# Performance work log

Hardware: AMD Instinct MI355X
Metric: run time of the kernel (lower is better)

## Reference

```python
import jax, jax.numpy as jnp
import numpy as np

M, N, D = 8, 50000, 256  # n_relations, nodes, d_model


def setup_inputs() -> dict:
    key = jax.random.key(0)
    ks = jax.random.split(key, 6)
    s = 0.02
    return {
        "zs": jax.random.normal(ks[0], (M, N, D), jnp.float32),
        # W_beta: Linear(M*D -> M), stored as [in, out]
        "Wb": jax.random.normal(ks[1], (M * D, M), jnp.float32) * s,
        "bb": jnp.zeros((M,), jnp.float32),
        # per-relation Linear(D -> D) stacks, stored [M, in, out]
        "Wmax": jax.random.normal(ks[2], (M, D, D), jnp.float32) * s,
        "bmax": jnp.zeros((M, D), jnp.float32),
        "Wphi": jax.random.normal(ks[3], (M, D, D), jnp.float32) * s,
        "bphi": jnp.zeros((M, D), jnp.float32),
        # W_c: Linear(3D -> D)
        "Wc": jax.random.normal(ks[4], (3 * D, D), jnp.float32) * s,
        "bc": jnp.zeros((D,), jnp.float32),
        # LayerNorm affine params
        "gamma": jnp.ones((D,), jnp.float32),
        "beta": jnp.zeros((D,), jnp.float32),
    }


def reference(zs, Wb, bb, Wmax, bmax, Wphi, bphi, Wc, bc, gamma, beta):
    Mr, Nn, Dd = zs.shape
    # --- sum branch: gated softmax mixture over relations ---
    cat = jnp.transpose(zs, (1, 0, 2)).reshape(Nn, Mr * Dd)  # [N, M*D] (no pad: M == n_max)
    gate = jax.nn.softmax(cat @ Wb + bb, axis=-1)            # [N, M]
    z_sum = jnp.einsum('nm,mnd->nd', gate, zs)               # [N, D]
    # --- max branch: per-relation linear then elementwise max over relations ---
    proj = jnp.einsum('mnd,mde->mne', zs, Wmax) + bmax[:, None, :]  # [M, N, D]
    z_max = proj.max(axis=0)
    # --- agr branch: sum_{i<j} phi_i*phi_j = 0.5*((sum phi)^2 - sum phi^2) ---
    phis = jnp.einsum('mnd,mde->mne', zs, Wphi) + bphi[:, None, :]  # [M, N, D]
    s1 = phis.sum(axis=0)
    z_agr = 0.5 * (s1 * s1 - (phis * phis).sum(axis=0))
    # --- combine + LayerNorm ---
    z = jnp.concatenate([z_sum, z_max, z_agr], axis=-1) @ Wc + bc   # [N, D]
    mu = z.mean(axis=-1, keepdims=True)
    var = z.var(axis=-1, keepdims=True)
    return (z - mu) / jnp.sqrt(var + 1e-5) * gamma + beta
```

## Files before the change

### kernel.cpp

```cpp
#include <hip/hip_runtime.h>

typedef unsigned short u16;
typedef unsigned int   u32;
typedef __attribute__((ext_vector_type(8))) __bf16 bf16x8;
typedef __attribute__((ext_vector_type(4))) float  f32x4;

#define MREL  8
#define DDIM  256
#define TROWS 32

#define WPHI_B 1024
#define WB_B   2048
#define WC_B   2112
#define NBLK   2496

__device__ __forceinline__ u16 f2bf(float x) {
  u32 u = __float_as_uint(x);
  u += 0x7fffu + ((u >> 16) & 1u);
  return (u16)(u >> 16);
}
__device__ __forceinline__ float bf2f(u16 x) {
  return __uint_as_float((u32)x << 16);
}

union U16x8 { u16 u[8]; uint4 q; bf16x8 v; };

#define SLOT(q, lr, ks) ((q)*16 + ((((lr) ^ (ks)) ^ ((q) << 1)) & 15))

#define MFMA16 __builtin_amdgcn_mfma_f32_16x16x32_bf16

#define BARRIER() do { \
  asm volatile("s_waitcnt lgkmcnt(0)" ::: "memory"); \
  __builtin_amdgcn_s_barrier(); \
  asm volatile("" ::: "memory"); \
} while (0)

__global__ __launch_bounds__(256) void swizzle_kernel(
    const float* __restrict__ Wmax, const float* __restrict__ Wphi,
    const float* __restrict__ Wb,   const float* __restrict__ Wc,
    u16* __restrict__ ws)
{
  int sb   = blockIdx.x * 4 + (threadIdx.x >> 6);
  int lane = threadIdx.x & 63;
  int quad = lane >> 4, c16 = lane & 15;
  U16x8 o;
  if (sb < WB_B) {
    const float* W = (sb < WPHI_B) ? Wmax : Wphi;
    int b = sb & 1023;
    int m = b >> 7, r = b & 127;
    int ct = r >> 3, ks = r & 7;
    const float* src = W + ((size_t)m * DDIM + (size_t)(ks * 32 + quad * 8)) * DDIM
                         + ct * 16 + c16;
    #pragma unroll
    for (int j = 0; j < 8; ++j) o.u[j] = f2bf(src[j * DDIM]);
  } else if (sb < WC_B) {
    int ksg = sb - WB_B;
    int kbase = ksg * 32 + quad * 8;
    if (c16 < 8) {
      #pragma unroll
      for (int j = 0; j < 8; ++j) o.u[j] = f2bf(Wb[(size_t)(kbase + j) * 8 + c16]);
    } else {
      o.q = make_uint4(0, 0, 0, 0);
    }
  } else {
    int r = sb - WC_B;
    int ct = r / 24, ks = r % 24;
    const float* src = Wc + (size_t)(ks * 32 + quad * 8) * DDIM + ct * 16 + c16;
    #pragma unroll
    for (int j = 0; j < 8; ++j) o.u[j] = f2bf(src[j * DDIM]);
  }
  *(uint4*)(ws + (size_t)sb * 512 + lane * 8) = o.q;
}

__global__ __launch_bounds__(512, 2) void fused_kernel(
    const float* __restrict__ zs,   const float* __restrict__ bb,
    const float* __restrict__ bmax, const float* __restrict__ bphi,
    const float* __restrict__ bc,   const float* __restrict__ gma,
    const float* __restrict__ bta,  const u16* __restrict__ ws,
    float* __restrict__ out, int N)
{
  const int tid  = threadIdx.x;
  const int lane = tid & 63;
  const int w    = tid >> 6;
  const int quad = lane >> 4;
  const int c16  = lane & 15;
  const int n0   = blockIdx.x * TROWS;
  const int st_row = tid >> 4;
  const int t15    = tid & 15;

  __shared__ __align__(16) u16 s_tile[MREL * 8192];
  __shared__ float s_lpart[8][TROWS][8];
  __shared__ float s_gate[TROWS][8];
  __shared__ float s_ln1[TROWS][8];
  __shared__ float s_ln2[TROWS][8];
  __shared__ float s_mrs[TROWS][2];

  const f32x4 vz = {0.f, 0.f, 0.f, 0.f};
  f32x4 zmx[2][2], s1v[2][2], s2v[2][2];
  #pragma unroll
  for (int rt = 0; rt < 2; ++rt)
    #pragma unroll
    for (int ct = 0; ct < 2; ++ct) {
      zmx[rt][ct] = (f32x4){-3e38f, -3e38f, -3e38f, -3e38f};
      s1v[rt][ct] = vz; s2v[rt][ct] = vz;
    }
  f32x4 lf0 = vz, lf1 = vz;

  const int g_row = n0 + st_row;
  const int st_lr = st_row & 15, st_rt = st_row >> 4;
  const float* zbase = zs + (size_t)g_row * DDIM + t15 * 4;

  float4 Fa[4], Fb[4];
  auto issue = [&](int m, float4* F) {
    if (g_row < N) {
      const float* p = zbase + (size_t)m * N * DDIM;
      #pragma unroll
      for (int k = 0; k < 4; ++k) F[k] = *(const float4*)(p + k * 64);
    } else {
      #pragma unroll
      for (int k = 0; k < 4; ++k) F[k] = make_float4(0.f, 0.f, 0.f, 0.f);
    }
  };
  auto wtile = [&](int m, const float4* F) {
    u16* tile = s_tile + m * 8192;
    #pragma unroll
    for (int k = 0; k < 4; ++k) {
      int c0 = k * 64 + t15 * 4;
      int ks = c0 >> 5, q = (c0 >> 3) & 3, j = c0 & 7;
      u32 lo = (u32)f2bf(F[k].x) | ((u32)f2bf(F[k].y) << 16);
      u32 hi = (u32)f2bf(F[k].z) | ((u32)f2bf(F[k].w) << 16);
      *(uint2*)(tile + (st_rt * 8 + ks) * 512 + SLOT(q, st_lr, ks) * 8 + j) =
          make_uint2(lo, hi);
    }
  };

  auto compute = [&](int m) {
    const u16* tile = s_tile + m * 8192;
    float bm0 = bmax[m * DDIM + (w * 2 + 0) * 16 + c16];
    float bm1 = bmax[m * DDIM + (w * 2 + 1) * 16 + c16];
    float bp0 = bphi[m * DDIM + (w * 2 + 0) * 16 + c16];
    float bp1 = bphi[m * DDIM + (w * 2 + 1) * 16 + c16];
    {
      U16x8 bg, a0, a1;
      bg.q = *(const uint4*)(ws + (size_t)(WB_B + m * 8 + w) * 512 + lane * 8);
      int so = SLOT(quad, c16, w) * 8;
      a0.q = *(const uint4*)(tile + w * 512 + so);
      a1.q = *(const uint4*)(tile + (8 + w) * 512 + so);
      lf0 = MFMA16(a0.v, bg.v, lf0, 0, 0, 0);
      lf1 = MFMA16(a1.v, bg.v, lf1, 0, 0, 0);
    }
    f32x4 pa[2][2];
    #pragma unroll
    for (int rt = 0; rt < 2; ++rt)
      #pragma unroll
      for (int ct = 0; ct < 2; ++ct) pa[rt][ct] = vz;
    {
      uint4 B[8][2];
      #pragma unroll
      for (int ks = 0; ks < 8; ++ks) {
        B[ks][0] = *(const uint4*)(ws + (size_t)(m * 128 + (w * 2 + 0) * 8 + ks) * 512 + lane * 8);
        B[ks][1] = *(const uint4*)(ws + (size_t)(m * 128 + (w * 2 + 1) * 8 + ks) * 512 + lane * 8);
      }
      #pragma unroll
      for (int ks = 0; ks < 8; ++ks) {
        U16x8 a0, a1, b0, b1;
        int so = SLOT(quad, c16, ks) * 8;
        a0.q = *(const uint4*)(tile + ks * 512 + so);
        a1.q = *(const uint4*)(tile + (8 + ks) * 512 + so);
        b0.q = B[ks][0]; b1.q = B[ks][1];
        pa[0][0] = MFMA16(a0.v, b0.v, pa[0][0], 0, 0, 0);
        pa[0][1] = MFMA16(a0.v, b1.v, pa[0][1], 0, 0, 0);
        pa[1][0] = MFMA16(a1.v, b0.v, pa[1][0], 0, 0, 0);
        pa[1][1] = MFMA16(a1.v, b1.v, pa[1][1], 0, 0, 0);
      }
      #pragma unroll
      for (int rt = 0; rt < 2; ++rt)
        #pragma unroll
        for (int r = 0; r < 4; ++r) {
          zmx[rt][0][r] = fmaxf(zmx[rt][0][r], pa[rt][0][r] + bm0);
          zmx[rt][1][r] = fmaxf(zmx[rt][1][r], pa[rt][1][r] + bm1);
        }
    }
    #pragma unroll
    for (int rt = 0; rt < 2; ++rt)
      #pragma unroll
      for (int ct = 0; ct < 2; ++ct) pa[rt][ct] = vz;
    {
      uint4 B[8][2];
      #pragma unroll
      for (int ks = 0; ks < 8; ++ks) {
        B[ks][0] = *(const uint4*)(ws + (size_t)(WPHI_B + m * 128 + (w * 2 + 0) * 8 + ks) * 512 + lane * 8);
        B[ks][1] = *(const uint4*)(ws + (size_t)(WPHI_B + m * 128 + (w * 2 + 1) * 8 + ks) * 512 + lane * 8);
      }
      #pragma unroll
      for (int ks = 0; ks < 8; ++ks) {
        U16x8 a0, a1, b0, b1;
        int so = SLOT(quad, c16, ks) * 8;
        a0.q = *(const uint4*)(tile + ks * 512 + so);
        a1.q = *(const uint4*)(tile + (8 + ks) * 512 + so);
        b0.q = B[ks][0]; b1.q = B[ks][1];
        pa[0][0] = MFMA16(a0.v, b0.v, pa[0][0], 0, 0, 0);
        pa[0][1] = MFMA16(a0.v, b1.v, pa[0][1], 0, 0, 0);
        pa[1][0] = MFMA16(a1.v, b0.v, pa[1][0], 0, 0, 0);
        pa[1][1] = MFMA16(a1.v, b1.v, pa[1][1], 0, 0, 0);
      }
      #pragma unroll
      for (int rt = 0; rt < 2; ++rt)
        #pragma unroll
        for (int r = 0; r < 4; ++r) {
          float v0 = pa[rt][0][r] + bp0;
          float v1 = pa[rt][1][r] + bp1;
          s1v[rt][0][r] += v0; s2v[rt][0][r] += v0 * v0;
          s1v[rt][1][r] += v1; s2v[rt][1][r] += v1 * v1;
        }
    }
  };

  issue(0, Fa);
  for (int m = 0; m < MREL; m += 2) {
    issue(m + 1, Fb);
    wtile(m, Fa);
    BARRIER();
    compute(m);
    if (m + 2 < MREL) issue(m + 2, Fa);
    wtile(m + 1, Fb);
    BARRIER();
    compute(m + 1);
  }

  if (c16 < 8) {
    #pragma unroll
    for (int r = 0; r < 4; ++r) {
      s_lpart[w][quad * 4 + r][c16]      = lf0[r];
      s_lpart[w][16 + quad * 4 + r][c16] = lf1[r];
    }
  }
  __syncthreads();
  if (tid < TROWS) {
    float lg[8]; float mx = -1e30f;
    #pragma unroll
    for (int mm = 0; mm < 8; ++mm) {
      float v = bb[mm];
      #pragma unroll
      for (int ww = 0; ww < 8; ++ww) v += s_lpart[ww][tid][mm];
      lg[mm] = v; mx = fmaxf(mx, v);
    }
    float s = 0.f;
    #pragma unroll
    for (int mm = 0; mm < 8; ++mm) { lg[mm] = __expf(lg[mm] - mx); s += lg[mm]; }
    float inv = 1.f / s;
    #pragma unroll
    for (int mm = 0; mm < 8; ++mm) s_gate[tid][mm] = lg[mm] * inv;
  }
  __syncthreads();

  float zsum[16];
  #pragma unroll
  for (int i = 0; i < 16; ++i) zsum[i] = 0.f;
  const int z_ks = t15 >> 1;
  const int z_q0 = (t15 & 1) * 2;
  const int z_base = (st_rt * 8 + z_ks) * 512;
  const int z_so0 = z_base + SLOT(z_q0, st_lr, z_ks) * 8;
  const int z_so1 = z_base + SLOT(z_q0 + 1, st_lr, z_ks) * 8;
  #pragma unroll
  for (int m = 0; m < MREL; ++m) {
    float g = s_gate[st_row][m];
    const u16* tile = s_tile + m * 8192;
    U16x8 v0, v1;
    v0.q = *(const uint4*)(tile + z_so0);
    v1.q = *(const uint4*)(tile + z_so1);
    #pragma unroll
    for (int j = 0; j < 8; ++j) {
      zsum[j]     += g * bf2f(v0.u[j]);
      zsum[8 + j] += g * bf2f(v1.u[j]);
    }
  }
  __syncthreads();

  {
    U16x8 p0, p1;
    #pragma unroll
    for (int j = 0; j < 8; ++j) { p0.u[j] = f2bf(zsum[j]); p1.u[j] = f2bf(zsum[8 + j]); }
    *(uint4*)(s_tile + z_so0) = p0.q;
    *(uint4*)(s_tile + z_so1) = p1.q;
  }
  #pragma unroll
  for (int ct = 0; ct < 2; ++ct) {
    int col = (w * 2 + ct) * 16 + c16;
    int ks = col >> 5, q = (col >> 3) & 3, j = col & 7;
    #pragma unroll
    for (int rt = 0; rt < 2; ++rt)
      #pragma unroll
      for (int r = 0; r < 4; ++r) {
        int lr = quad * 4 + r;
        s_tile[8192 + (rt * 8 + ks) * 512 + SLOT(q, lr, ks) * 8 + j] = f2bf(zmx[rt][ct][r]);
      }
  }
  #pragma unroll
  for (int ct = 0; ct < 2; ++ct) {
    int col = (w * 2 + ct) * 16 + c16;
    int ks = col >> 5, q = (col >> 3) & 3, j = col & 7;
    #pragma unroll
    for (int rt = 0; rt < 2; ++rt)
      #pragma unroll
      for (int r = 0; r < 4; ++r) {
        int lr = quad * 4 + r;
        float za = 0.5f * (s1v[rt][ct][r] * s1v[rt][ct][r] - s2v[rt][ct][r]);
        s_tile[16384 + (rt * 8 + ks) * 512 + SLOT(q, lr, ks) * 8 + j] = f2bf(za);
      }
  }
  __syncthreads();

  f32x4 oc[2][2];
  #pragma unroll
  for (int rt = 0; rt < 2; ++rt)
    #pragma unroll
    for (int ct = 0; ct < 2; ++ct) oc[rt][ct] = vz;
  #pragma unroll
  for (int p = 0; p < 3; ++p) {
    const u16* pb = s_tile + p * 8192;
    uint4 B[8][2];
    #pragma unroll
    for (int ks = 0; ks < 8; ++ks) {
      B[ks][0] = *(const uint4*)(ws + (size_t)(WC_B + (w * 2 + 0) * 24 + p * 8 + ks) * 512 + lane * 8);
      B[ks][1] = *(const uint4*)(ws + (size_t)(WC_B + (w * 2 + 1) * 24 + p * 8 + ks) * 512 + lane * 8);
    }
    #pragma unroll
    for (int ks = 0; ks < 8; ++ks) {
      U16x8 a0, a1, b0, b1;
      int so = SLOT(quad, c16, ks) * 8;
      a0.q = *(const uint4*)(pb + ks * 512 + so);
      a1.q = *(const uint4*)(pb + (8 + ks) * 512 + so);
      b0.q = B[ks][0]; b1.q = B[ks][1];
      oc[0][0] = MFMA16(a0.v, b0.v, oc[0][0], 0, 0, 0);
      oc[0][1] = MFMA16(a0.v, b1.v, oc[0][1], 0, 0, 0);
      oc[1][0] = MFMA16(a1.v, b0.v, oc[1][0], 0, 0, 0);
      oc[1][1] = MFMA16(a1.v, b1.v, oc[1][1], 0, 0, 0);
    }
  }

  #pragma unroll
  for (int ct = 0; ct < 2; ++ct) {
    float bcv = bc[(w * 2 + ct) * 16 + c16];
    #pragma unroll
    for (int rt = 0; rt < 2; ++rt)
      #pragma unroll
      for (int r = 0; r < 4; ++r) oc[rt][ct][r] += bcv;
  }
  float ps[2][4], pss[2][4];
  #pragma unroll
  for (int rt = 0; rt < 2; ++rt)
    #pragma unroll
    for (int r = 0; r < 4; ++r) {
      float a = oc[rt][0][r], b = oc[rt][1][r];
      ps[rt][r]  = a + b;
      pss[rt][r] = a * a + b * b;
    }
  #pragma unroll
  for (int off = 1; off < 16; off <<= 1) {
    #pragma unroll
    for (int rt = 0; rt < 2; ++rt)
      #pragma unroll
      for (int r = 0; r < 4; ++r) {
        ps[rt][r]  += __shfl_xor(ps[rt][r], off);
        pss[rt][r] += __shfl_xor(pss[rt][r], off);
      }
  }
  if (c16 == 0) {
    #pragma unroll
    for (int rt = 0; rt < 2; ++rt)
      #pragma unroll
      for (int r = 0; r < 4; ++r) s_ln1[rt * 16 + quad * 4 + r][w] = ps[rt][r];
  }
  if (c16 == 1) {
    #pragma unroll
    for (int rt = 0; rt < 2; ++rt)
      #pragma unroll
      for (int r = 0; r < 4; ++r) s_ln2[rt * 16 + quad * 4 + r][w] = pss[rt][r];
  }
  __syncthreads();
  if (tid < TROWS) {
    float s = 0.f, ss = 0.f;
    #pragma unroll
    for (int ww = 0; ww < 8; ++ww) { s += s_ln1[tid][ww]; ss += s_ln2[tid][ww]; }
    float mu  = s * (1.0f / 256.0f);
    float var = ss * (1.0f / 256.0f) - mu * mu;
    s_mrs[tid][0] = mu;
    s_mrs[tid][1] = rsqrtf(var + 1e-5f);
  }
  __syncthreads();
  #pragma unroll
  for (int ct = 0; ct < 2; ++ct) {
    int col = (w * 2 + ct) * 16 + c16;
    float g = gma[col], b = bta[col];
    #pragma unroll
    for (int rt = 0; rt < 2; ++rt)
      #pragma unroll
      for (int r = 0; r < 4; ++r) {
        int row = rt * 16 + quad * 4 + r;
        int grow = n0 + row;
        if (grow < N) {
          float mu = s_mrs[row][0], rs = s_mrs[row][1];
          out[(size_t)grow * DDIM + col] = (oc[rt][ct][r] - mu) * rs * g + b;
        }
      }
  }
}

extern "C" void kernel_launch(void* const* d_in, const int* in_sizes, int n_in,
                              void* d_out, int out_size, void* d_ws, size_t ws_size,
                              hipStream_t stream) {
  const float* zs   = (const float*)d_in[0];
  const float* Wb   = (const float*)d_in[1];
  const float* bb   = (const float*)d_in[2];
  const float* Wmax = (const float*)d_in[3];
  const float* bmax = (const float*)d_in[4];
  const float* Wphi = (const float*)d_in[5];
  const float* bphi = (const float*)d_in[6];
  const float* Wc   = (const float*)d_in[7];
  const float* bc   = (const float*)d_in[8];
  const float* gma  = (const float*)d_in[9];
  const float* bta  = (const float*)d_in[10];
  float* out = (float*)d_out;
  u16* ws = (u16*)d_ws;

  int N = in_sizes[0] / (MREL * DDIM);

  swizzle_kernel<<<NBLK / 4, 256, 0, stream>>>(Wmax, Wphi, Wb, Wc, ws);
  int grid = (N + TROWS - 1) / TROWS;
  fused_kernel<<<grid, 512, 0, stream>>>(zs, bb, bmax, bphi, bc, gma, bta, ws, out, N);
}
```

Measured before the change: 813.9 us.

## Double block to 1024 threads, one column tile per wave, move prefetch into compute

The fused kernel now runs 16 waves per block instead of 8. Each wave owns one 16-column output tile instead of two, which halves per-thread accumulators and B-fragment registers. The staging loads become 32 bytes per thread with a single 16-byte LDS store, and the next relation's global load is issued inside compute after the Wphi fragments are fetched, to overlap latency. LDS use per block is unchanged, so occupancy is still limited by shared memory. The extra waves give more latency hiding, but also add barrier cost and duplicate B-fragment loads across more waves.

```diff
diff --git a/kernel.cpp b/kernel.cpp
--- a/kernel.cpp
+++ b/kernel.cpp
@@ -72,7 +72,7 @@
   *(uint4*)(ws + (size_t)sb * 512 + lane * 8) = o.q;
 }
 
-__global__ __launch_bounds__(512, 2) void fused_kernel(
+__global__ __launch_bounds__(1024, 4) void fused_kernel(
     const float* __restrict__ zs,   const float* __restrict__ bb,
     const float* __restrict__ bmax, const float* __restrict__ bphi,
     const float* __restrict__ bc,   const float* __restrict__ gma,
@@ -85,62 +85,56 @@
   const int quad = lane >> 4;
   const int c16  = lane & 15;
   const int n0   = blockIdx.x * TROWS;
-  const int st_row = tid >> 4;
-  const int t15    = tid & 15;
+  const int st_row = tid >> 5;
+  const int s32    = tid & 31;
 
   __shared__ __align__(16) u16 s_tile[MREL * 8192];
   __shared__ float s_lpart[8][TROWS][8];
   __shared__ float s_gate[TROWS][8];
-  __shared__ float s_ln1[TROWS][8];
-  __shared__ float s_ln2[TROWS][8];
+  __shared__ float s_ln1[TROWS][16];
+  __shared__ float s_ln2[TROWS][16];
   __shared__ float s_mrs[TROWS][2];
 
   const f32x4 vz = {0.f, 0.f, 0.f, 0.f};
-  f32x4 zmx[2][2], s1v[2][2], s2v[2][2];
-  #pragma unroll
-  for (int rt = 0; rt < 2; ++rt)
-    #pragma unroll
-    for (int ct = 0; ct < 2; ++ct) {
-      zmx[rt][ct] = (f32x4){-3e38f, -3e38f, -3e38f, -3e38f};
-      s1v[rt][ct] = vz; s2v[rt][ct] = vz;
-    }
+  f32x4 zmx[2], s1v[2], s2v[2];
+  #pragma unroll
+  for (int rt = 0; rt < 2; ++rt) {
+    zmx[rt] = (f32x4){-3e38f, -3e38f, -3e38f, -3e38f};
+    s1v[rt] = vz; s2v[rt] = vz;
+  }
   f32x4 lf0 = vz, lf1 = vz;
 
   const int g_row = n0 + st_row;
   const int st_lr = st_row & 15, st_rt = st_row >> 4;
-  const float* zbase = zs + (size_t)g_row * DDIM + t15 * 4;
-
-  float4 Fa[4], Fb[4];
+  const int st_ks = s32 >> 2, st_q = s32 & 3;
+  const int st_off = (st_rt * 8 + st_ks) * 512 + SLOT(st_q, st_lr, st_ks) * 8;
+  const float* zbase = zs + (size_t)g_row * DDIM + s32 * 8;
+
+  float4 Fa[2], Fb[2];
   auto issue = [&](int m, float4* F) {
     if (g_row < N) {
       const float* p = zbase + (size_t)m * N * DDIM;
-      #pragma unroll
-      for (int k = 0; k < 4; ++k) F[k] = *(const float4*)(p + k * 64);
+      F[0] = *(const float4*)p;
+      F[1] = *(const float4*)(p + 4);
     } else {
-      #pragma unroll
-      for (int k = 0; k < 4; ++k) F[k] = make_float4(0.f, 0.f, 0.f, 0.f);
+      F[0] = make_float4(0.f, 0.f, 0.f, 0.f);
+      F[1] = make_float4(0.f, 0.f, 0.f, 0.f);
     }
   };
   auto wtile = [&](int m, const float4* F) {
-    u16* tile = s_tile + m * 8192;
-    #pragma unroll
-    for (int k = 0; k < 4; ++k) {
-      int c0 = k * 64 + t15 * 4;
-      int ks = c0 >> 5, q = (c0 >> 3) & 3, j = c0 & 7;
-      u32 lo = (u32)f2bf(F[k].x) | ((u32)f2bf(F[k].y) << 16);
-      u32 hi = (u32)f2bf(F[k].z) | ((u32)f2bf(F[k].w) << 16);
-      *(uint2*)(tile + (st_rt * 8 + ks) * 512 + SLOT(q, st_lr, ks) * 8 + j) =
-          make_uint2(lo, hi);
-    }
+    U16x8 pk;
+    pk.u[0] = f2bf(F[0].x); pk.u[1] = f2bf(F[0].y);
+    pk.u[2] = f2bf(F[0].z); pk.u[3] = f2bf(F[0].w);
+    pk.u[4] = f2bf(F[1].x); pk.u[5] = f2bf(F[1].y);
+    pk.u[6] = f2bf(F[1].z); pk.u[7] = f2bf(F[1].w);
+    *(uint4*)(s_tile + m * 8192 + st_off) = pk.q;
   };
 
-  auto compute = [&](int m) {
+  auto compute = [&](int m, int mnext, float4* Fn) {
     const u16* tile = s_tile + m * 8192;
-    float bm0 = bmax[m * DDIM + (w * 2 + 0) * 16 + c16];
-    float bm1 = bmax[m * DDIM + (w * 2 + 1) * 16 + c16];
-    float bp0 = bphi[m * DDIM + (w * 2 + 0) * 16 + c16];
-    float bp1 = bphi[m * DDIM + (w * 2 + 1) * 16 + c16];
-    {
+    float bm = bmax[m * DDIM + w * 16 + c16];
+    float bp = bphi[m * DDIM + w * 16 + c16];
+    if (w < 8) {
       U16x8 bg, a0, a1;
       bg.q = *(const uint4*)(ws + (size_t)(WB_B + m * 8 + w) * 512 + lane * 8);
       int so = SLOT(quad, c16, w) * 8;
@@ -149,86 +143,67 @@
       lf0 = MFMA16(a0.v, bg.v, lf0, 0, 0, 0);
       lf1 = MFMA16(a1.v, bg.v, lf1, 0, 0, 0);
     }
-    f32x4 pa[2][2];
-    #pragma unroll
-    for (int rt = 0; rt < 2; ++rt)
-      #pragma unroll
-      for (int ct = 0; ct < 2; ++ct) pa[rt][ct] = vz;
+    f32x4 p0, p1;
+    p0 = vz; p1 = vz;
     {
-      uint4 B[8][2];
+      uint4 B[8];
+      #pragma unroll
+      for (int ks = 0; ks < 8; ++ks)
+        B[ks] = *(const uint4*)(ws + (size_t)(m * 128 + w * 8 + ks) * 512 + lane * 8);
       #pragma unroll
       for (int ks = 0; ks < 8; ++ks) {
-        B[ks][0] = *(const uint4*)(ws + (size_t)(m * 128 + (w * 2 + 0) * 8 + ks) * 512 + lane * 8);
-        B[ks][1] = *(const uint4*)(ws + (size_t)(m * 128 + (w * 2 + 1) * 8 + ks) * 512 + lane * 8);
-      }
-      #pragma unroll
-      for (int ks = 0; ks < 8; ++ks) {
-        U16x8 a0, a1, b0, b1;
+        U16x8 a0, a1, b;
         int so = SLOT(quad, c16, ks) * 8;
         a0.q = *(const uint4*)(tile + ks * 512 + so);
         a1.q = *(const uint4*)(tile + (8 + ks) * 512 + so);
-        b0.q = B[ks][0]; b1.q = B[ks][1];
-        pa[0][0] = MFMA16(a0.v, b0.v, pa[0][0], 0, 0, 0);
-        pa[0][1] = MFMA16(a0.v, b1.v, pa[0][1], 0, 0, 0);
-        pa[1][0] = MFMA16(a1.v, b0.v, pa[1][0], 0, 0, 0);
-        pa[1][1] = MFMA16(a1.v, b1.v, pa[1][1], 0, 0, 0);
-      }
-      #pragma unroll
-      for (int rt = 0; rt < 2; ++rt)
-        #pragma unroll
-        for (int r = 0; r < 4; ++r) {
-          zmx[rt][0][r] = fmaxf(zmx[rt][0][r], pa[rt][0][r] + bm0);
-          zmx[rt][1][r] = fmaxf(zmx[rt][1][r], pa[rt][1][r] + bm1);
-        }
-    }
-    #pragma unroll
-    for (int rt = 0; rt < 2; ++rt)
-      #pragma unroll
-      for (int ct = 0; ct < 2; ++ct) pa[rt][ct] = vz;
+        b.q = B[ks];
+        p0 = MFMA16(a0.v, b.v, p0, 0, 0, 0);
+        p1 = MFMA16(a1.v, b.v, p1, 0, 0, 0);
+      }
+      #pragma unroll
+      for (int r = 0; r < 4; ++r) {
+        zmx[0][r] = fmaxf(zmx[0][r], p0[r] + bm);
+        zmx[1][r] = fmaxf(zmx[1][r], p1[r] + bm);
+      }
+    }
+    p0 = vz; p1 = vz;
     {
-      uint4 B[8][2];
+      uint4 B[8];
+      #pragma unroll
+      for (int ks = 0; ks < 8; ++ks)
+        B[ks] = *(const uint4*)(ws + (size_t)(WPHI_B + m * 128 + w * 8 + ks) * 512 + lane * 8);
+      if (mnext >= 0) issue(mnext, Fn);
       #pragma unroll
       for (int ks = 0; ks < 8; ++ks) {
-        B[ks][0] = *(const uint4*)(ws + (size_t)(WPHI_B + m * 128 + (w * 2 + 0) * 8 + ks) * 512 + lane * 8);
-        B[ks][1] = *(const uint4*)(ws + (size_t)(WPHI_B + m * 128 + (w * 2 + 1) * 8 + ks) * 512 + lane * 8);
-      }
-      #pragma unroll
-      for (int ks = 0; ks < 8; ++ks) {
-        U16x8 a0, a1, b0, b1;
+        U16x8 a0, a1, b;
         int so = SLOT(quad, c16, ks) * 8;
         a0.q = *(const uint4*)(tile + ks * 512 + so);
         a1.q = *(const uint4*)(tile + (8 + ks) * 512 + so);
-        b0.q = B[ks][0]; b1.q = B[ks][1];
-        pa[0][0] = MFMA16(a0.v, b0.v, pa[0][0], 0, 0, 0);
-        pa[0][1] = MFMA16(a0.v, b1.v, pa[0][1], 0, 0, 0);
-        pa[1][0] = MFMA16(a1.v, b0.v, pa[1][0], 0, 0, 0);
-        pa[1][1] = MFMA16(a1.v, b1.v, pa[1][1], 0, 0, 0);
-      }
-      #pragma unroll
-      for (int rt = 0; rt < 2; ++rt)
-        #pragma unroll
-        for (int r = 0; r < 4; ++r) {
-          float v0 = pa[rt][0][r] + bp0;
-          float v1 = pa[rt][1][r] + bp1;
-          s1v[rt][0][r] += v0; s2v[rt][0][r] += v0 * v0;
-          s1v[rt][1][r] += v1; s2v[rt][1][r] += v1 * v1;
-        }
+        b.q = B[ks];
+        p0 = MFMA16(a0.v, b.v, p0, 0, 0, 0);
+        p1 = MFMA16(a1.v, b.v, p1, 0, 0, 0);
+      }
+      #pragma unroll
+      for (int r = 0; r < 4; ++r) {
+        float v0 = p0[r] + bp;
+        float v1 = p1[r] + bp;
+        s1v[0][r] += v0; s2v[0][r] += v0 * v0;
+        s1v[1][r] += v1; s2v[1][r] += v1 * v1;
+      }
     }
   };
 
   issue(0, Fa);
   for (int m = 0; m < MREL; m += 2) {
-    issue(m + 1, Fb);
     wtile(m, Fa);
     BARRIER();
-    compute(m);
-    if (m + 2 < MREL) issue(m + 2, Fa);
+    compute(m, m + 1, Fb);
     wtile(m + 1, Fb);
     BARRIER();
-    compute(m + 1);
-  }
-
-  if (c16 < 8) {
+    compute(m + 1, (m + 2 < MREL) ? m + 2 : -1, Fa);
+  }
+
+  if (w < 8 && c16 < 8) {
     #pragma unroll
     for (int r = 0; r < 4; ++r) {
       s_lpart[w][quad * 4 + r][c16]      = lf0[r];
@@ -254,108 +229,71 @@
   }
   __syncthreads();
 
-  float zsum[16];
-  #pragma unroll
-  for (int i = 0; i < 16; ++i) zsum[i] = 0.f;
-  const int z_ks = t15 >> 1;
-  const int z_q0 = (t15 & 1) * 2;
-  const int z_base = (st_rt * 8 + z_ks) * 512;
-  const int z_so0 = z_base + SLOT(z_q0, st_lr, z_ks) * 8;
-  const int z_so1 = z_base + SLOT(z_q0 + 1, st_lr, z_ks) * 8;
+  float zsum[8];
+  #pragma unroll
+  for (int i = 0; i < 8; ++i) zsum[i] = 0.f;
   #pragma unroll
   for (int m = 0; m < MREL; ++m) {
     float g = s_gate[st_row][m];
-    const u16* tile = s_tile + m * 8192;
-    U16x8 v0, v1;
-    v0.q = *(const uint4*)(tile + z_so0);
-    v1.q = *(const uint4*)(tile + z_so1);
-    #pragma unroll
-    for (int j = 0; j < 8; ++j) {
-      zsum[j]     += g * bf2f(v0.u[j]);
-      zsum[8 + j] += g * bf2f(v1.u[j]);
-    }
+    U16x8 v;
+    v.q = *(const uint4*)(s_tile + m * 8192 + st_off);
+    #pragma unroll
+    for (int j = 0; j < 8; ++j) zsum[j] += g * bf2f(v.u[j]);
   }
   __syncthreads();
 
   {
-    U16x8 p0, p1;
-    #pragma unroll
-    for (int j = 0; j < 8; ++j) { p0.u[j] = f2bf(zsum[j]); p1.u[j] = f2bf(zsum[8 + j]); }
-    *(uint4*)(s_tile + z_so0) = p0.q;
-    *(uint4*)(s_tile + z_so1) = p1.q;
-  }
-  #pragma unroll
-  for (int ct = 0; ct < 2; ++ct) {
-    int col = (w * 2 + ct) * 16 + c16;
+    U16x8 pk;
+    #pragma unroll
+    for (int j = 0; j < 8; ++j) pk.u[j] = f2bf(zsum[j]);
+    *(uint4*)(s_tile + st_off) = pk.q;
+  }
+  {
+    int col = w * 16 + c16;
     int ks = col >> 5, q = (col >> 3) & 3, j = col & 7;
     #pragma unroll
     for (int rt = 0; rt < 2; ++rt)
       #pragma unroll
       for (int r = 0; r < 4; ++r) {
         int lr = quad * 4 + r;
-        s_tile[8192 + (rt * 8 + ks) * 512 + SLOT(q, lr, ks) * 8 + j] = f2bf(zmx[rt][ct][r]);
-      }
-  }
-  #pragma unroll
-  for (int ct = 0; ct < 2; ++ct) {
-    int col = (w * 2 + ct) * 16 + c16;
-    int ks = col >> 5, q = (col >> 3) & 3, j = col & 7;
-    #pragma unroll
-    for (int rt = 0; rt < 2; ++rt)
-      #pragma unroll
-      for (int r = 0; r < 4; ++r) {
-        int lr = quad * 4 + r;
-        float za = 0.5f * (s1v[rt][ct][r] * s1v[rt][ct][r] - s2v[rt][ct][r]);
+        s_tile[8192 + (rt * 8 + ks) * 512 + SLOT(q, lr, ks) * 8 + j] = f2bf(zmx[rt][r]);
+        float za = 0.5f * (s1v[rt][r] * s1v[rt][r] - s2v[rt][r]);
         s_tile[16384 + (rt * 8 + ks) * 512 + SLOT(q, lr, ks) * 8 + j] = f2bf(za);
       }
   }
   __syncthreads();
 
-  f32x4 oc[2][2];
-  #pragma unroll
-  for (int rt = 0; rt < 2; ++rt)
-    #pragma unroll
-    for (int ct = 0; ct < 2; ++ct) oc[rt][ct] = vz;
+  f32x4 oc0 = vz, oc1 = vz;
   #pragma unroll
   for (int p = 0; p < 3; ++p) {
     const u16* pb = s_tile + p * 8192;
-    uint4 B[8][2];
+    uint4 B[8];
+    #pragma unroll
+    for (int ks = 0; ks < 8; ++ks)
+      B[ks] = *(const uint4*)(ws + (size_t)(WC_B + w * 24 + p * 8 + ks) * 512 + lane * 8);
     #pragma unroll
     for (int ks = 0; ks < 8; ++ks) {
-      B[ks][0] = *(const uint4*)(ws + (size_t)(WC_B + (w * 2 + 0) * 24 + p * 8 + ks) * 512 + lane * 8);
-      B[ks][1] = *(const uint4*)(ws + (size_t)(WC_B + (w * 2 + 1) * 24 + p * 8 + ks) * 512 + lane * 8);
-    }
-    #pragma unroll
-    for (int ks = 0; ks < 8; ++ks) {
-      U16x8 a0, a1, b0, b1;
+      U16x8 a0, a1, b;
       int so = SLOT(quad, c16, ks) * 8;
       a0.q = *(const uint4*)(pb + ks * 512 + so);
       a1.q = *(const uint4*)(pb + (8 + ks) * 512 + so);
-      b0.q = B[ks][0]; b1.q = B[ks][1];
-      oc[0][0] = MFMA16(a0.v, b0.v, oc[0][0], 0, 0, 0);
-      oc[0][1] = MFMA16(a0.v, b1.v, oc[0][1], 0, 0, 0);
-      oc[1][0] = MFMA16(a1.v, b0.v, oc[1][0], 0, 0, 0);
-      oc[1][1] = MFMA16(a1.v, b1.v, oc[1][1], 0, 0, 0);
-    }
-  }
-
-  #pragma unroll
-  for (int ct = 0; ct < 2; ++ct) {
-    float bcv = bc[(w * 2 + ct) * 16 + c16];
-    #pragma unroll
-    for (int rt = 0; rt < 2; ++rt)
-      #pragma unroll
-      for (int r = 0; r < 4; ++r) oc[rt][ct][r] += bcv;
+      b.q = B[ks];
+      oc0 = MFMA16(a0.v, b.v, oc0, 0, 0, 0);
+      oc1 = MFMA16(a1.v, b.v, oc1, 0, 0, 0);
+    }
+  }
+
+  {
+    float bcv = bc[w * 16 + c16];
+    #pragma unroll
+    for (int r = 0; r < 4; ++r) { oc0[r] += bcv; oc1[r] += bcv; }
   }
   float ps[2][4], pss[2][4];
   #pragma unroll
-  for (int rt = 0; rt < 2; ++rt)
-    #pragma unroll
-    for (int r = 0; r < 4; ++r) {
-      float a = oc[rt][0][r], b = oc[rt][1][r];
-      ps[rt][r]  = a + b;
-      pss[rt][r] = a * a + b * b;
-    }
+  for (int r = 0; r < 4; ++r) {
+    ps[0][r] = oc0[r]; pss[0][r] = oc0[r] * oc0[r];
+    ps[1][r] = oc1[r]; pss[1][r] = oc1[r] * oc1[r];
+  }
   #pragma unroll
   for (int off = 1; off < 16; off <<= 1) {
     #pragma unroll
@@ -382,16 +320,15 @@
   if (tid < TROWS) {
     float s = 0.f, ss = 0.f;
     #pragma unroll
-    for (int ww = 0; ww < 8; ++ww) { s += s_ln1[tid][ww]; ss += s_ln2[tid][ww]; }
+    for (int ww = 0; ww < 16; ++ww) { s += s_ln1[tid][ww]; ss += s_ln2[tid][ww]; }
     float mu  = s * (1.0f / 256.0f);
     float var = ss * (1.0f / 256.0f) - mu * mu;
     s_mrs[tid][0] = mu;
     s_mrs[tid][1] = rsqrtf(var + 1e-5f);
   }
   __syncthreads();
-  #pragma unroll
-  for (int ct = 0; ct < 2; ++ct) {
-    int col = (w * 2 + ct) * 16 + c16;
+  {
+    int col = w * 16 + c16;
     float g = gma[col], b = bta[col];
     #pragma unroll
     for (int rt = 0; rt < 2; ++rt)
@@ -401,7 +338,8 @@
         int grow = n0 + row;
         if (grow < N) {
           float mu = s_mrs[row][0], rs = s_mrs[row][1];
-          out[(size_t)grow * DDIM + col] = (oc[rt][ct][r] - mu) * rs * g + b;
+          float v = (rt == 0) ? oc0[r] : oc1[r];
+          out[(size_t)grow * DDIM + col] = (v - mu) * rs * g + b;
         }
       }
   }
@@ -428,5 +366,5 @@
 
   swizzle_kernel<<<NBLK / 4, 256, 0, stream>>>(Wmax, Wphi, Wb, Wc, ws);
   int grid = (N + TROWS - 1) / TROWS;
-  fused_kernel<<<grid, 512, 0, stream>>>(zs, bb, bmax, bphi, bc, gma, bta, ws, out, N);
-}
+  fused_kernel<<<grid, 1024, 0, stream>>>(zs, bb, bmax, bphi, bc, gma, bta, ws, out, N);
+}
```

New measurement: 1.457 ms. +79.0%, slower.
